# Optimization experiments

Hardware: AMD Instinct MI355X
Metric: run time of the kernel (lower is better)

## Reference

```python
import jax, jax.numpy as jnp
import numpy as np

B, T, D = 2, 2048, 1024
H = 16
HD = D // H  # 64
A = 16
MLP_H = 4 * D
EPS = 1e-6


def rmsnorm(x, w):
    # x: [..., C], w: [C]
    return x * jax.lax.rsqrt(jnp.mean(x * x, axis=-1, keepdims=True) + EPS) * w


def setup_inputs() -> dict:
    key = jax.random.key(0)
    ks = jax.random.split(key, 24)
    s = 0.02
    inp = {
        'x': jax.random.normal(ks[0], (B, T, D), jnp.float32),
        'actions': jax.random.normal(ks[1], (B, T, A), jnp.float32),
        # block norms
        'n1_w': jnp.ones((D,), jnp.float32),
        'n2_w': jnp.ones((D,), jnp.float32),
        # attention projections (stored [in, out])
        'q_w': jax.random.normal(ks[2], (D, D), jnp.float32) * s,
        'q_b': jnp.zeros((D,), jnp.float32),
        'k_w': jax.random.normal(ks[3], (D, D), jnp.float32) * s,
        'k_b': jnp.zeros((D,), jnp.float32),
        'v_w': jax.random.normal(ks[4], (D, D), jnp.float32) * s,
        'v_b': jnp.zeros((D,), jnp.float32),
        'qn_w': jnp.ones((HD,), jnp.float32),
        'kn_w': jnp.ones((HD,), jnp.float32),
        'o_w': jax.random.normal(ks[5], (D, D), jnp.float32) * s,
        'o_b': jnp.zeros((D,), jnp.float32),
        # action conditioning
        'ae1_w': jax.random.normal(ks[6], (A, D), jnp.float32) * s,
        'ae1_b': jnp.zeros((D,), jnp.float32),
        'ae2_w': jax.random.normal(ks[7], (D, D), jnp.float32) * s,
        'ae2_b': jnp.zeros((D,), jnp.float32),
        'mod_w': jax.random.normal(ks[8], (D, 4 * D), jnp.float32) * s,
        'mod_b': jnp.zeros((4 * D,), jnp.float32),
        # mlp
        'm1_w': jax.random.normal(ks[9], (D, MLP_H), jnp.float32) * s,
        'm1_b': jnp.zeros((MLP_H,), jnp.float32),
        'm2_w': jax.random.normal(ks[10], (MLP_H, D), jnp.float32) * s,
        'm2_b': jnp.zeros((D,), jnp.float32),
    }
    return inp


def _forward(x, actions, n1_w, n2_w, q_w, q_b, k_w, k_b, v_w, v_b, qn_w, kn_w,
             o_w, o_b, ae1_w, ae1_b, ae2_w, ae2_b, mod_w, mod_b,
             m1_w, m1_b, m2_w, m2_b):
    Bc, Tc, Dc = x.shape
    scale = HD ** -0.5

    # --- causal temporal attention with QK RMSNorm ---
    h = rmsnorm(x, n1_w)
    q = (h @ q_w + q_b).reshape(Bc, Tc, H, HD).transpose(0, 2, 1, 3)  # [B,H,T,hd]
    k = (h @ k_w + k_b).reshape(Bc, Tc, H, HD).transpose(0, 2, 1, 3)
    v = (h @ v_w + v_b).reshape(Bc, Tc, H, HD).transpose(0, 2, 1, 3)
    q = rmsnorm(q, qn_w)
    k = rmsnorm(k, kn_w)
    attn = jnp.einsum('bhqd,bhkd->bhqk', q, k) * scale
    causal = jnp.triu(jnp.ones((Tc, Tc), bool), k=1)  # True above diagonal -> masked
    attn = jnp.where(causal, -jnp.inf, attn)
    attn = jax.nn.softmax(attn, axis=-1)
    out = jnp.einsum('bhqk,bhkd->bhqd', attn, v)
    out = out.transpose(0, 2, 1, 3).reshape(Bc, Tc, Dc)
    x = x + (out @ o_w + o_b)

    # --- action conditioning (AdaLN-style; eval mode, no dropout) ---
    ae = jax.nn.silu(actions @ ae1_w + ae1_b) @ ae2_w + ae2_b  # [B,T,D]
    mod = jax.nn.silu(ae) @ mod_w + mod_b  # [B,T,4D]
    shift1, scale1, _, _ = jnp.split(mod, 4, axis=-1)
    x = x * (1.0 + scale1) + shift1

    # --- MLP ---
    h2 = rmsnorm(x, n2_w)
    x = x + (jax.nn.gelu(h2 @ m1_w + m1_b, approximate=False) @ m2_w + m2_b)
    return x


def reference(x, actions, n1_w, n2_w, q_w, q_b, k_w, k_b, v_w, v_b, qn_w, kn_w,
              o_w, o_b, ae1_w, ae1_b, ae2_w, ae2_b, mod_w, mod_b,
              m1_w, m1_b, m2_w, m2_b):
    return _forward(x, actions, n1_w, n2_w, q_w, q_b, k_w, k_b, v_w, v_b,
                    qn_w, kn_w, o_w, o_b, ae1_w, ae1_b, ae2_w, ae2_b,
                    mod_w, mod_b, m1_w, m1_b, m2_w, m2_b)
```

## Files before the change

kernel.cpp:

```cpp
#include <hip/hip_runtime.h>
#include <hip/hip_bf16.h>
#include <math.h>

typedef __hip_bfloat16 bf16;
typedef __attribute__((ext_vector_type(8))) short short8;
typedef __attribute__((ext_vector_type(4))) float float4_;

#define B_   2
#define T_   2048
#define D_   1024
#define H_   16
#define NTOK (B_ * T_)
#define NEG_SENT -1e30f

#define AS1 __attribute__((address_space(1)))
#define AS3 __attribute__((address_space(3)))

static __device__ __forceinline__ float b2f(bf16 v) { return __bfloat162float(v); }
static __device__ __forceinline__ bf16  f2b(float v) { return __float2bfloat16(v); }
static __device__ __forceinline__ short f2s(float v) {
    unsigned u = __builtin_bit_cast(unsigned, v);
    unsigned r = (u + 0x7FFFu + ((u >> 16) & 1u)) >> 16;
    return (short)r;
}
static __device__ __forceinline__ float to_f(float v) { return v; }
static __device__ __forceinline__ float to_f(bf16 v) { return __bfloat162float(v); }
static __device__ __forceinline__ void  store_o(float* p, float v) { *p = v; }
static __device__ __forceinline__ void  store_o(bf16* p, float v) { *p = __float2bfloat16(v); }
static __device__ __forceinline__ void gl_lds16(const void* g, void* l) {
    __builtin_amdgcn_global_load_lds((const AS1 unsigned int*)g, (AS3 unsigned int*)l, 16, 0, 0);
}

__global__ __launch_bounds__(256) void rmsnorm_k(const float* __restrict__ x,
                                                 const float* __restrict__ w,
                                                 bf16* __restrict__ out) {
    int t = blockIdx.x, tid = threadIdx.x;
    float xs[4], ss = 0.f;
#pragma unroll
    for (int i = 0; i < 4; ++i) {
        float v = x[(size_t)t * D_ + tid + i * 256];
        xs[i] = v; ss += v * v;
    }
    __shared__ float red[4];
#pragma unroll
    for (int off = 32; off > 0; off >>= 1) ss += __shfl_xor(ss, off, 64);
    if ((tid & 63) == 0) red[tid >> 6] = ss;
    __syncthreads();
    ss = red[0] + red[1] + red[2] + red[3];
    float inv = rsqrtf(ss * (1.f / D_) + 1e-6f);
#pragma unroll
    for (int i = 0; i < 4; ++i) {
        int c = tid + i * 256;
        out[(size_t)t * D_ + c] = f2b(xs[i] * inv * w[c]);
    }
}

__global__ __launch_bounds__(256) void modnorm_k(float* __restrict__ x1,
                                                 const bf16* __restrict__ mod,
                                                 const float* __restrict__ w,
                                                 bf16* __restrict__ h2) {
    int t = blockIdx.x, tid = threadIdx.x;
    float xs[4], ss = 0.f;
#pragma unroll
    for (int i = 0; i < 4; ++i) {
        int c = tid + i * 256;
        float sh = b2f(mod[(size_t)t * 2048 + c]);
        float sc = b2f(mod[(size_t)t * 2048 + 1024 + c]);
        float v = x1[(size_t)t * D_ + c] * (1.f + sc) + sh;
        xs[i] = v; ss += v * v;
        x1[(size_t)t * D_ + c] = v;
    }
    __shared__ float red[4];
#pragma unroll
    for (int off = 32; off > 0; off >>= 1) ss += __shfl_xor(ss, off, 64);
    if ((tid & 63) == 0) red[tid >> 6] = ss;
    __syncthreads();
    ss = red[0] + red[1] + red[2] + red[3];
    float inv = rsqrtf(ss * (1.f / D_) + 1e-6f);
#pragma unroll
    for (int i = 0; i < 4; ++i) {
        int c = tid + i * 256;
        h2[(size_t)t * D_ + c] = f2b(xs[i] * inv * w[c]);
    }
}

__global__ __launch_bounds__(256) void ae1_k(const float* __restrict__ actions,
                                             const float* __restrict__ w,
                                             const float* __restrict__ b,
                                             bf16* __restrict__ out) {
    int t = blockIdx.x, tid = threadIdx.x;
    float av[16];
#pragma unroll
    for (int a = 0; a < 16; ++a) av[a] = actions[(size_t)t * 16 + a];
#pragma unroll
    for (int i = 0; i < 4; ++i) {
        int n = tid + i * 256;
        float acc = b[n];
#pragma unroll
        for (int a = 0; a < 16; ++a) acc += av[a] * w[a * D_ + n];
        out[(size_t)t * D_ + n] = f2b(acc / (1.f + expf(-acc)));
    }
}

struct WD { const float* src; bf16* dst; int K, N, ldw, tiles; };
struct WPack { WD d[8]; };
__global__ __launch_bounds__(256) void wprep_k(WPack p) {
    int bid = blockIdx.x;
    int mi = 0, cum = 0;
#pragma unroll
    for (mi = 0; mi < 8; ++mi) {
        if (bid < cum + p.d[mi].tiles) break;
        cum += p.d[mi].tiles;
    }
    if (mi >= 8) return;
    WD w = p.d[mi];
    int local = bid - cum;
    int tilesK = w.K >> 6;
    int tk = local % tilesK, tn = local / tilesK;
    int k0 = tk * 64, n0 = tn * 64;
    __shared__ short Tt[64 * 72];
    int t = threadIdx.x;
    int row = t >> 2, seg = t & 3;
    const float* sp = w.src + (size_t)(k0 + row) * w.ldw + n0 + seg * 16;
#pragma unroll
    for (int q = 0; q < 4; ++q) {
        float4_ f = *(const float4_*)(sp + q * 4);
#pragma unroll
        for (int j = 0; j < 4; ++j) Tt[(seg * 16 + q * 4 + j) * 72 + row] = f2s(f[j]);
    }
    __syncthreads();
    bf16* dp = w.dst + (size_t)(n0 + row) * w.K + k0 + seg * 16;
    *(short8*)dp       = *(const short8*)&Tt[row * 72 + seg * 16];
    *(short8*)(dp + 8) = *(const short8*)&Tt[row * 72 + seg * 16 + 8];
}

__global__ __launch_bounds__(256) void bcat_k(const float* __restrict__ qb,
                                              const float* __restrict__ kb,
                                              const float* __restrict__ vb,
                                              float* __restrict__ dst) {
    int i = blockIdx.x * 256 + threadIdx.x;
    const float* s = (i < 1024) ? qb : (i < 2048) ? kb : vb;
    dst[i] = s[i & 1023];
}

template <int ACT, int QKN, typename ResT, typename OutT>
__global__ __launch_bounds__(256) void gemm_k(const bf16* __restrict__ A,
                                              const bf16* __restrict__ Bt,
                                              const float* __restrict__ bias,
                                              const ResT* __restrict__ res,
                                              OutT* __restrict__ out,
                                              int M, int N, int K, int ldo,
                                              const float* __restrict__ qn_w,
                                              const float* __restrict__ kn_w) {
    __shared__ __align__(16) short As[128 * 64];
    __shared__ __align__(16) short Bs[128 * 64];
    const int tid = threadIdx.x;
    const int bm = blockIdx.y * 128, bn = blockIdx.x * 128;
    const int wave = tid >> 6, lane = tid & 63;
    const int wm = (wave & 1) * 64, wn = (wave >> 1) * 64;
    const int l15 = lane & 15, quad = lane >> 4;
    const int lrow = lane >> 3, lseg = (lane & 7) * 8;
    float4_ acc[4][4] = {};

    for (int k0 = 0; k0 < K; k0 += 64) {
#pragma unroll
        for (int it = 0; it < 4; ++it) {
            int r = it * 32 + wave * 8;
            gl_lds16((const short*)A + (size_t)(bm + r + lrow) * K + k0 + lseg, &As[r * 64]);
            gl_lds16((const short*)Bt + (size_t)(bn + r + lrow) * K + k0 + lseg, &Bs[r * 64]);
        }
        __syncthreads();
#pragma unroll
        for (int kk = 0; kk < 64; kk += 32) {
            short8 af[4], bfr[4];
#pragma unroll
            for (int i = 0; i < 4; ++i)
                af[i] = *(const short8*)&As[(wm + i * 16 + l15) * 64 + kk + quad * 8];
#pragma unroll
            for (int j = 0; j < 4; ++j)
                bfr[j] = *(const short8*)&Bs[(wn + j * 16 + l15) * 64 + kk + quad * 8];
#pragma unroll
            for (int i = 0; i < 4; ++i)
#pragma unroll
                for (int j = 0; j < 4; ++j)
                    acc[i][j] = __builtin_amdgcn_mfma_f32_16x16x32_bf16(af[i], bfr[j], acc[i][j], 0, 0, 0);
        }
        __syncthreads();
    }

    int seg = (bn + wn) >> 10;
    float nwv[4];
    if (QKN && seg < 2) {
        const float* nw = seg ? kn_w : qn_w;
#pragma unroll
        for (int j = 0; j < 4; ++j) nwv[j] = nw[j * 16 + l15];
    }

#pragma unroll
    for (int i = 0; i < 4; ++i) {
        float vv[4][4];
#pragma unroll
        for (int j = 0; j < 4; ++j) {
            float bv = bias[bn + wn + j * 16 + l15];
#pragma unroll
            for (int r = 0; r < 4; ++r) vv[j][r] = acc[i][j][r] + bv;
        }
        if (QKN && seg < 2) {
#pragma unroll
            for (int r = 0; r < 4; ++r) {
                float ss = vv[0][r] * vv[0][r] + vv[1][r] * vv[1][r]
                         + vv[2][r] * vv[2][r] + vv[3][r] * vv[3][r];
#pragma unroll
                for (int off = 8; off > 0; off >>= 1) ss += __shfl_xor(ss, off, 16);
                float inv = rsqrtf(ss * (1.f / 64.f) + 1e-6f);
#pragma unroll
                for (int j = 0; j < 4; ++j) vv[j][r] *= inv * nwv[j];
            }
        }
#pragma unroll
        for (int j = 0; j < 4; ++j) {
            int col = bn + wn + j * 16 + l15;
#pragma unroll
            for (int r = 0; r < 4; ++r) {
                int row = bm + wm + i * 16 + quad * 4 + r;
                float v = vv[j][r];
                if (ACT == 1) v = v / (1.f + expf(-v));
                else if (ACT == 2) v = 0.5f * v * (1.f + erff(v * 0.70710678118654752f));
                if (res) v += to_f(res[(size_t)row * ldo + col]);
                store_o(&out[(size_t)row * ldo + col], v);
            }
        }
    }
}

template <int ACT, typename ResT, typename OutT>
__global__ __launch_bounds__(256) void gemm64_k(const bf16* __restrict__ A,
                                                const bf16* __restrict__ Bt,
                                                const float* __restrict__ bias,
                                                const ResT* __restrict__ res,
                                                OutT* __restrict__ out,
                                                int M, int N, int K) {
    __shared__ __align__(16) short As[64 * 64];
    __shared__ __align__(16) short Bs[128 * 64];
    const int tid = threadIdx.x;
    const int bm = blockIdx.y * 64, bn = blockIdx.x * 128;
    const int wave = tid >> 6, lane = tid & 63;
    const int wm = (wave & 1) * 32, wn = (wave >> 1) * 64;
    const int l15 = lane & 15, quad = lane >> 4;
    const int lrow = lane >> 3, lseg = (lane & 7) * 8;
    float4_ acc[2][4] = {};

    for (int k0 = 0; k0 < K; k0 += 64) {
#pragma unroll
        for (int it = 0; it < 2; ++it) {
            int r = wave * 16 + it * 8;
            gl_lds16((const short*)A + (size_t)(bm + r + lrow) * K + k0 + lseg, &As[r * 64]);
        }
#pragma unroll
        for (int it = 0; it < 4; ++it) {
            int r = it * 32 + wave * 8;
            gl_lds16((const short*)Bt + (size_t)(bn + r + lrow) * K + k0 + lseg, &Bs[r * 64]);
        }
        __syncthreads();
#pragma unroll
        for (int kk = 0; kk < 64; kk += 32) {
            short8 af[2], bfr[4];
#pragma unroll
            for (int i = 0; i < 2; ++i)
                af[i] = *(const short8*)&As[(wm + i * 16 + l15) * 64 + kk + quad * 8];
#pragma unroll
            for (int j = 0; j < 4; ++j)
                bfr[j] = *(const short8*)&Bs[(wn + j * 16 + l15) * 64 + kk + quad * 8];
#pragma unroll
            for (int i = 0; i < 2; ++i)
#pragma unroll
                for (int j = 0; j < 4; ++j)
                    acc[i][j] = __builtin_amdgcn_mfma_f32_16x16x32_bf16(af[i], bfr[j], acc[i][j], 0, 0, 0);
        }
        __syncthreads();
    }

#pragma unroll
    for (int i = 0; i < 2; ++i)
#pragma unroll
        for (int j = 0; j < 4; ++j) {
            int col = bn + wn + j * 16 + l15;
            float bv = bias[col];
#pragma unroll
            for (int r = 0; r < 4; ++r) {
                int row = bm + wm + i * 16 + quad * 4 + r;
                float v = acc[i][j][r] + bv;
                if (ACT == 1) v = v / (1.f + expf(-v));
                else if (ACT == 2) v = 0.5f * v * (1.f + erff(v * 0.70710678118654752f));
                if (res) v += to_f(res[(size_t)row * N + col]);
                store_o(&out[(size_t)row * N + col], v);
            }
        }
}

__global__ __launch_bounds__(256) void attn_k(const bf16* __restrict__ QKV,
                                              bf16* __restrict__ O) {
    __shared__ __align__(16) short Vt[2][64 * 72];
    __shared__ __align__(16) short Ps[4][16 * 72];
    const int bh = blockIdx.y, b = bh >> 4, h = bh & 15;
    const int q0 = T_ - 64 * (blockIdx.x + 1);
    const int tid = threadIdx.x, wave = tid >> 6, lane = tid & 63;
    const int l15 = lane & 15, quad = lane >> 4;
    const size_t base = (size_t)b * T_ * 3072 + h * 64;
    const short* Qp = (const short*)QKV + base;
    const short* Kp = Qp + 1024;
    const short* Vp = Qp + 2048;

    const int qrow = q0 + wave * 16 + l15;
    short8 qf0 = *(const short8*)(Qp + (size_t)qrow * 3072 + quad * 8);
    short8 qf1 = *(const short8*)(Qp + (size_t)qrow * 3072 + 32 + quad * 8);

    float4_ oacc[4] = {};
    float l_r[4] = {0.f, 0.f, 0.f, 0.f};

    const int vrow = tid >> 2, vseg = tid & 3;
    const int nit = q0 / 64 + 1;

    {
        const short* vp = Vp + (size_t)vrow * 3072 + vseg * 16;
        short8 v0 = *(const short8*)vp;
        short8 v1 = *(const short8*)(vp + 8);
#pragma unroll
        for (int j = 0; j < 8; ++j) Vt[0][(vseg * 16 + j) * 72 + vrow] = v0[j];
#pragma unroll
        for (int j = 0; j < 8; ++j) Vt[0][(vseg * 16 + 8 + j) * 72 + vrow] = v1[j];
    }
    __syncthreads();

    for (int it = 0; it < nit; ++it) {
        const int kv0 = it * 64, buf = it & 1;
        if (it + 1 < nit) {
            const short* vp = Vp + (size_t)(kv0 + 64 + vrow) * 3072 + vseg * 16;
            short8 v0 = *(const short8*)vp;
            short8 v1 = *(const short8*)(vp + 8);
#pragma unroll
            for (int j = 0; j < 8; ++j) Vt[buf ^ 1][(vseg * 16 + j) * 72 + vrow] = v0[j];
#pragma unroll
            for (int j = 0; j < 8; ++j) Vt[buf ^ 1][(vseg * 16 + 8 + j) * 72 + vrow] = v1[j];
        }

        float4_ s[4];
#pragma unroll
        for (int c = 0; c < 4; ++c) {
            const short* kp = Kp + (size_t)(kv0 + c * 16 + l15) * 3072 + quad * 8;
            short8 kb0 = *(const short8*)kp;
            short8 kb1 = *(const short8*)(kp + 32);
            float4_ sc = {};
            sc = __builtin_amdgcn_mfma_f32_16x16x32_bf16(qf0, kb0, sc, 0, 0, 0);
            sc = __builtin_amdgcn_mfma_f32_16x16x32_bf16(qf1, kb1, sc, 0, 0, 0);
            s[c] = sc;
        }

#pragma unroll
        for (int r = 0; r < 4; ++r) {
            int qr = q0 + wave * 16 + quad * 4 + r;
#pragma unroll
            for (int c = 0; c < 4; ++c) {
                int kvi = kv0 + c * 16 + l15;
                float val = (kvi > qr) ? NEG_SENT : s[c][r] * 0.125f;
                float p = __expf(val);
                s[c][r] = p;
                l_r[r] += p;
            }
        }

#pragma unroll
        for (int c = 0; c < 4; ++c)
#pragma unroll
            for (int r = 0; r < 4; ++r)
                Ps[wave][(quad * 4 + r) * 72 + c * 16 + l15] = f2s(s[c][r]);

#pragma unroll
        for (int kk = 0; kk < 64; kk += 32) {
            short8 pf = *(const short8*)&Ps[wave][l15 * 72 + kk + quad * 8];
#pragma unroll
            for (int d = 0; d < 4; ++d) {
                short8 vf = *(const short8*)&Vt[buf][(d * 16 + l15) * 72 + kk + quad * 8];
                oacc[d] = __builtin_amdgcn_mfma_f32_16x16x32_bf16(pf, vf, oacc[d], 0, 0, 0);
            }
        }
        __syncthreads();
    }

    float linv[4];
#pragma unroll
    for (int r = 0; r < 4; ++r) {
        float l = l_r[r];
#pragma unroll
        for (int off = 8; off > 0; off >>= 1) l += __shfl_xor(l, off, 16);
        linv[r] = 1.f / l;
    }
#pragma unroll
    for (int d = 0; d < 4; ++d)
#pragma unroll
        for (int r = 0; r < 4; ++r) {
            int qr = q0 + wave * 16 + quad * 4 + r;
            O[(size_t)(b * T_ + qr) * D_ + h * 64 + d * 16 + l15] = f2b(oacc[d][r] * linv[r]);
        }
}

extern "C" void kernel_launch(void* const* d_in, const int* in_sizes, int n_in,
                              void* d_out, int out_size, void* d_ws, size_t ws_size,
                              hipStream_t stream) {
    const float* x     = (const float*)d_in[0];
    const float* acts  = (const float*)d_in[1];
    const float* n1_w  = (const float*)d_in[2];
    const float* n2_w  = (const float*)d_in[3];
    const float* q_w   = (const float*)d_in[4];
    const float* q_b   = (const float*)d_in[5];
    const float* k_w   = (const float*)d_in[6];
    const float* k_b   = (const float*)d_in[7];
    const float* v_w   = (const float*)d_in[8];
    const float* v_b   = (const float*)d_in[9];
    const float* qn_w  = (const float*)d_in[10];
    const float* kn_w  = (const float*)d_in[11];
    const float* o_w   = (const float*)d_in[12];
    const float* o_b   = (const float*)d_in[13];
    const float* ae1_w = (const float*)d_in[14];
    const float* ae1_b = (const float*)d_in[15];
    const float* ae2_w = (const float*)d_in[16];
    const float* ae2_b = (const float*)d_in[17];
    const float* mod_w = (const float*)d_in[18];
    const float* mod_b = (const float*)d_in[19];
    const float* m1_w  = (const float*)d_in[20];
    const float* m1_b  = (const float*)d_in[21];
    const float* m2_w  = (const float*)d_in[22];
    const float* m2_b  = (const float*)d_in[23];
    float* out = (float*)d_out;

    char* ws = (char*)d_ws;
    const size_t MB = 1ull << 20;
    bf16*  Ah   = (bf16*)(ws + 0);
    bf16*  QKVp = (bf16*)(ws + 8 * MB);
    bf16*  AO   = (bf16*)(ws + 32 * MB);
    bf16*  AE1  = (bf16*)(ws + 8 * MB);
    bf16*  AES  = (bf16*)(ws + 16 * MB);
    bf16*  MOD  = (bf16*)(ws + 24 * MB);
    bf16*  M1G  = (bf16*)(ws + 8 * MB);
    float* X1   = out;

    bf16* WTqkv = (bf16*)(ws + 40 * MB);
    bf16* WTo   = (bf16*)(ws + 46 * MB);
    bf16* WTae2 = (bf16*)(ws + 48 * MB);
    bf16* WTmod = (bf16*)(ws + 50 * MB);
    bf16* WTm1  = (bf16*)(ws + 54 * MB);
    bf16* WTm2  = (bf16*)(ws + 62 * MB);
    float* biasQKV = (float*)(ws + 70 * MB);

    dim3 blk(256);

    WPack p;
    p.d[0] = { q_w,   WTqkv,                1024, 1024, 1024, 256 };
    p.d[1] = { k_w,   WTqkv + 1024 * 1024,  1024, 1024, 1024, 256 };
    p.d[2] = { v_w,   WTqkv + 2048 * 1024,  1024, 1024, 1024, 256 };
    p.d[3] = { o_w,   WTo,   1024, 1024, 1024, 256 };
    p.d[4] = { ae2_w, WTae2, 1024, 1024, 1024, 256 };
    p.d[5] = { mod_w, WTmod, 1024, 2048, 4096, 512 };
    p.d[6] = { m1_w,  WTm1,  1024, 4096, 4096, 1024 };
    p.d[7] = { m2_w,  WTm2,  4096, 1024, 1024, 1024 };
    wprep_k<<<3840, blk, 0, stream>>>(p);
    bcat_k<<<12, blk, 0, stream>>>(q_b, k_b, v_b, biasQKV);

    rmsnorm_k<<<NTOK, blk, 0, stream>>>(x, n1_w, Ah);
    gemm_k<0, 1, float, bf16><<<dim3(24, 32), blk, 0, stream>>>(Ah, WTqkv, biasQKV, (const float*)nullptr, QKVp, NTOK, 3072, 1024, 3072, qn_w, kn_w);
    attn_k<<<dim3(T_ / 64, B_ * H_), blk, 0, stream>>>(QKVp, AO);
    gemm64_k<0, float, float><<<dim3(8, 64), blk, 0, stream>>>(AO, WTo, o_b, x, X1, NTOK, 1024, 1024);
    ae1_k<<<NTOK, blk, 0, stream>>>(acts, ae1_w, ae1_b, AE1);
    gemm64_k<1, float, bf16><<<dim3(8, 64), blk, 0, stream>>>(AE1, WTae2, ae2_b, (const float*)nullptr, AES, NTOK, 1024, 1024);
    gemm_k<0, 0, float, bf16><<<dim3(16, 32), blk, 0, stream>>>(AES, WTmod, mod_b, (const float*)nullptr, MOD, NTOK, 2048, 1024, 2048, nullptr, nullptr);
    modnorm_k<<<NTOK, blk, 0, stream>>>(X1, MOD, n2_w, Ah);
    gemm_k<2, 0, float, bf16><<<dim3(32, 32), blk, 0, stream>>>(Ah, WTm1, m1_b, (const float*)nullptr, M1G, NTOK, 4096, 1024, 4096, nullptr, nullptr);
    gemm64_k<0, float, float><<<dim3(8, 64), blk, 0, stream>>>(M1G, WTm2, m2_b, X1, out, NTOK, 1024, 4096);
}
```

Baseline: 594.1 us.

## Write V transposed from QKV GEMM and use single-wave attention blocks

The QKV GEMM epilogue now writes V directly in a head-major transposed layout [b,h,d,t] and Q/K into a 2048-wide buffer. The attention kernel drops its LDS transpose of V, double buffering and block syncs, and reads V fragments straight from global memory. It also switches to one 64-thread wave per 16 query rows, giving four times as many blocks. This removes the in-kernel transpose and barrier cost, but V is now reloaded from global/L2 by each wave instead of being shared through LDS across four waves.

```diff
diff --git a/kernel.cpp b/kernel.cpp
--- a/kernel.cpp
+++ b/kernel.cpp
@@ -5,6 +5,7 @@
 typedef __hip_bfloat16 bf16;
 typedef __attribute__((ext_vector_type(8))) short short8;
 typedef __attribute__((ext_vector_type(4))) float float4_;
+typedef __attribute__((ext_vector_type(4))) unsigned short ushort4_;
 
 #define B_   2
 #define T_   2048
@@ -18,10 +19,10 @@
 
 static __device__ __forceinline__ float b2f(bf16 v) { return __bfloat162float(v); }
 static __device__ __forceinline__ bf16  f2b(float v) { return __float2bfloat16(v); }
-static __device__ __forceinline__ short f2s(float v) {
+static __device__ __forceinline__ unsigned short f2s(float v) {
     unsigned u = __builtin_bit_cast(unsigned, v);
     unsigned r = (u + 0x7FFFu + ((u >> 16) & 1u)) >> 16;
-    return (short)r;
+    return (unsigned short)r;
 }
 static __device__ __forceinline__ float to_f(float v) { return v; }
 static __device__ __forceinline__ float to_f(bf16 v) { return __bfloat162float(v); }
@@ -126,7 +127,7 @@
     for (int q = 0; q < 4; ++q) {
         float4_ f = *(const float4_*)(sp + q * 4);
 #pragma unroll
-        for (int j = 0; j < 4; ++j) Tt[(seg * 16 + q * 4 + j) * 72 + row] = f2s(f[j]);
+        for (int j = 0; j < 4; ++j) Tt[(seg * 16 + q * 4 + j) * 72 + row] = (short)f2s(f[j]);
     }
     __syncthreads();
     bf16* dp = w.dst + (size_t)(n0 + row) * w.K + k0 + seg * 16;
@@ -143,7 +144,7 @@
     dst[i] = s[i & 1023];
 }
 
-template <int ACT, int QKN, typename ResT, typename OutT>
+template <int ACT, int QKN, int VOUT, typename ResT, typename OutT>
 __global__ __launch_bounds__(256) void gemm_k(const bf16* __restrict__ A,
                                               const bf16* __restrict__ Bt,
                                               const float* __restrict__ bias,
@@ -151,7 +152,8 @@
                                               OutT* __restrict__ out,
                                               int M, int N, int K, int ldo,
                                               const float* __restrict__ qn_w,
-                                              const float* __restrict__ kn_w) {
+                                              const float* __restrict__ kn_w,
+                                              bf16* __restrict__ vt) {
     __shared__ __align__(16) short As[128 * 64];
     __shared__ __align__(16) short Bs[128 * 64];
     const int tid = threadIdx.x;
@@ -217,17 +219,29 @@
                 for (int j = 0; j < 4; ++j) vv[j][r] *= inv * nwv[j];
             }
         }
-#pragma unroll
-        for (int j = 0; j < 4; ++j) {
-            int col = bn + wn + j * 16 + l15;
-#pragma unroll
-            for (int r = 0; r < 4; ++r) {
-                int row = bm + wm + i * 16 + quad * 4 + r;
-                float v = vv[j][r];
-                if (ACT == 1) v = v / (1.f + expf(-v));
-                else if (ACT == 2) v = 0.5f * v * (1.f + erff(v * 0.70710678118654752f));
-                if (res) v += to_f(res[(size_t)row * ldo + col]);
-                store_o(&out[(size_t)row * ldo + col], v);
+        if (VOUT && seg >= 2) {
+#pragma unroll
+            for (int j = 0; j < 4; ++j) {
+                int col = bn + wn + j * 16 + l15 - 2048;
+                int hh = col >> 6, hd = col & 63;
+                int row0 = bm + wm + i * 16 + quad * 4;
+                int bb = row0 >> 11, t0 = row0 & 2047;
+                ushort4_ u = { f2s(vv[j][0]), f2s(vv[j][1]), f2s(vv[j][2]), f2s(vv[j][3]) };
+                *(ushort4_*)((unsigned short*)vt + ((size_t)((bb * 16 + hh) * 64 + hd)) * 2048 + t0) = u;
+            }
+        } else {
+#pragma unroll
+            for (int j = 0; j < 4; ++j) {
+                int col = bn + wn + j * 16 + l15;
+#pragma unroll
+                for (int r = 0; r < 4; ++r) {
+                    int row = bm + wm + i * 16 + quad * 4 + r;
+                    float v = vv[j][r];
+                    if (ACT == 1) v = v / (1.f + expf(-v));
+                    else if (ACT == 2) v = 0.5f * v * (1.f + erff(v * 0.70710678118654752f));
+                    if (res) v += to_f(res[(size_t)row * ldo + col]);
+                    store_o(&out[(size_t)row * ldo + col], v);
+                }
             }
         }
     }
@@ -298,56 +312,33 @@
         }
 }
 
-__global__ __launch_bounds__(256) void attn_k(const bf16* __restrict__ QKV,
-                                              bf16* __restrict__ O) {
-    __shared__ __align__(16) short Vt[2][64 * 72];
-    __shared__ __align__(16) short Ps[4][16 * 72];
+__global__ __launch_bounds__(64) void attn_k(const bf16* __restrict__ QK,
+                                             const bf16* __restrict__ VT,
+                                             bf16* __restrict__ O) {
+    __shared__ __align__(16) short Ps[16 * 72];
     const int bh = blockIdx.y, b = bh >> 4, h = bh & 15;
-    const int q0 = T_ - 64 * (blockIdx.x + 1);
-    const int tid = threadIdx.x, wave = tid >> 6, lane = tid & 63;
+    const int q0 = T_ - 16 * (blockIdx.x + 1);
+    const int lane = threadIdx.x;
     const int l15 = lane & 15, quad = lane >> 4;
-    const size_t base = (size_t)b * T_ * 3072 + h * 64;
-    const short* Qp = (const short*)QKV + base;
+    const short* Qp = (const short*)QK + (size_t)b * T_ * 2048 + h * 64;
     const short* Kp = Qp + 1024;
-    const short* Vp = Qp + 2048;
-
-    const int qrow = q0 + wave * 16 + l15;
-    short8 qf0 = *(const short8*)(Qp + (size_t)qrow * 3072 + quad * 8);
-    short8 qf1 = *(const short8*)(Qp + (size_t)qrow * 3072 + 32 + quad * 8);
+    const short* Vp = (const short*)VT + (size_t)(b * 16 + h) * 64 * 2048;
+
+    const int qrow = q0 + l15;
+    short8 qf0 = *(const short8*)(Qp + (size_t)qrow * 2048 + quad * 8);
+    short8 qf1 = *(const short8*)(Qp + (size_t)qrow * 2048 + 32 + quad * 8);
 
     float4_ oacc[4] = {};
     float l_r[4] = {0.f, 0.f, 0.f, 0.f};
-
-    const int vrow = tid >> 2, vseg = tid & 3;
     const int nit = q0 / 64 + 1;
 
-    {
-        const short* vp = Vp + (size_t)vrow * 3072 + vseg * 16;
-        short8 v0 = *(const short8*)vp;
-        short8 v1 = *(const short8*)(vp + 8);
-#pragma unroll
-        for (int j = 0; j < 8; ++j) Vt[0][(vseg * 16 + j) * 72 + vrow] = v0[j];
-#pragma unroll
-        for (int j = 0; j < 8; ++j) Vt[0][(vseg * 16 + 8 + j) * 72 + vrow] = v1[j];
-    }
-    __syncthreads();
-
     for (int it = 0; it < nit; ++it) {
-        const int kv0 = it * 64, buf = it & 1;
-        if (it + 1 < nit) {
-            const short* vp = Vp + (size_t)(kv0 + 64 + vrow) * 3072 + vseg * 16;
-            short8 v0 = *(const short8*)vp;
-            short8 v1 = *(const short8*)(vp + 8);
-#pragma unroll
-            for (int j = 0; j < 8; ++j) Vt[buf ^ 1][(vseg * 16 + j) * 72 + vrow] = v0[j];
-#pragma unroll
-            for (int j = 0; j < 8; ++j) Vt[buf ^ 1][(vseg * 16 + 8 + j) * 72 + vrow] = v1[j];
-        }
+        const int kv0 = it * 64;
 
         float4_ s[4];
 #pragma unroll
         for (int c = 0; c < 4; ++c) {
-            const short* kp = Kp + (size_t)(kv0 + c * 16 + l15) * 3072 + quad * 8;
+            const short* kp = Kp + (size_t)(kv0 + c * 16 + l15) * 2048 + quad * 8;
             short8 kb0 = *(const short8*)kp;
             short8 kb1 = *(const short8*)(kp + 32);
             float4_ sc = {};
@@ -358,7 +349,7 @@
 
 #pragma unroll
         for (int r = 0; r < 4; ++r) {
-            int qr = q0 + wave * 16 + quad * 4 + r;
+            int qr = q0 + quad * 4 + r;
 #pragma unroll
             for (int c = 0; c < 4; ++c) {
                 int kvi = kv0 + c * 16 + l15;
@@ -373,18 +364,17 @@
         for (int c = 0; c < 4; ++c)
 #pragma unroll
             for (int r = 0; r < 4; ++r)
-                Ps[wave][(quad * 4 + r) * 72 + c * 16 + l15] = f2s(s[c][r]);
+                Ps[(quad * 4 + r) * 72 + c * 16 + l15] = (short)f2s(s[c][r]);
 
 #pragma unroll
         for (int kk = 0; kk < 64; kk += 32) {
-            short8 pf = *(const short8*)&Ps[wave][l15 * 72 + kk + quad * 8];
+            short8 pf = *(const short8*)&Ps[l15 * 72 + kk + quad * 8];
 #pragma unroll
             for (int d = 0; d < 4; ++d) {
-                short8 vf = *(const short8*)&Vt[buf][(d * 16 + l15) * 72 + kk + quad * 8];
+                short8 vf = *(const short8*)(Vp + (size_t)(d * 16 + l15) * 2048 + kv0 + kk + quad * 8);
                 oacc[d] = __builtin_amdgcn_mfma_f32_16x16x32_bf16(pf, vf, oacc[d], 0, 0, 0);
             }
         }
-        __syncthreads();
     }
 
     float linv[4];
@@ -399,7 +389,7 @@
     for (int d = 0; d < 4; ++d)
 #pragma unroll
         for (int r = 0; r < 4; ++r) {
-            int qr = q0 + wave * 16 + quad * 4 + r;
+            int qr = q0 + quad * 4 + r;
             O[(size_t)(b * T_ + qr) * D_ + h * 64 + d * 16 + l15] = f2b(oacc[d][r] * linv[r]);
         }
 }
@@ -436,7 +426,8 @@
     char* ws = (char*)d_ws;
     const size_t MB = 1ull << 20;
     bf16*  Ah   = (bf16*)(ws + 0);
-    bf16*  QKVp = (bf16*)(ws + 8 * MB);
+    bf16*  QKp  = (bf16*)(ws + 8 * MB);
+    bf16*  VT   = (bf16*)(ws + 24 * MB);
     bf16*  AO   = (bf16*)(ws + 32 * MB);
     bf16*  AE1  = (bf16*)(ws + 8 * MB);
     bf16*  AES  = (bf16*)(ws + 16 * MB);
@@ -467,13 +458,13 @@
     bcat_k<<<12, blk, 0, stream>>>(q_b, k_b, v_b, biasQKV);
 
     rmsnorm_k<<<NTOK, blk, 0, stream>>>(x, n1_w, Ah);
-    gemm_k<0, 1, float, bf16><<<dim3(24, 32), blk, 0, stream>>>(Ah, WTqkv, biasQKV, (const float*)nullptr, QKVp, NTOK, 3072, 1024, 3072, qn_w, kn_w);
-    attn_k<<<dim3(T_ / 64, B_ * H_), blk, 0, stream>>>(QKVp, AO);
+    gemm_k<0, 1, 1, float, bf16><<<dim3(24, 32), blk, 0, stream>>>(Ah, WTqkv, biasQKV, (const float*)nullptr, QKp, NTOK, 3072, 1024, 2048, qn_w, kn_w, VT);
+    attn_k<<<dim3(T_ / 16, B_ * H_), dim3(64), 0, stream>>>(QKp, VT, AO);
     gemm64_k<0, float, float><<<dim3(8, 64), blk, 0, stream>>>(AO, WTo, o_b, x, X1, NTOK, 1024, 1024);
     ae1_k<<<NTOK, blk, 0, stream>>>(acts, ae1_w, ae1_b, AE1);
     gemm64_k<1, float, bf16><<<dim3(8, 64), blk, 0, stream>>>(AE1, WTae2, ae2_b, (const float*)nullptr, AES, NTOK, 1024, 1024);
-    gemm_k<0, 0, float, bf16><<<dim3(16, 32), blk, 0, stream>>>(AES, WTmod, mod_b, (const float*)nullptr, MOD, NTOK, 2048, 1024, 2048, nullptr, nullptr);
+    gemm_k<0, 0, 0, float, bf16><<<dim3(16, 32), blk, 0, stream>>>(AES, WTmod, mod_b, (const float*)nullptr, MOD, NTOK, 2048, 1024, 2048, nullptr, nullptr, nullptr);
     modnorm_k<<<NTOK, blk, 0, stream>>>(X1, MOD, n2_w, Ah);
-    gemm_k<2, 0, float, bf16><<<dim3(32, 32), blk, 0, stream>>>(Ah, WTm1, m1_b, (const float*)nullptr, M1G, NTOK, 4096, 1024, 4096, nullptr, nullptr);
+    gemm_k<2, 0, 0, float, bf16><<<dim3(32, 32), blk, 0, stream>>>(Ah, WTm1, m1_b, (const float*)nullptr, M1G, NTOK, 4096, 1024, 4096, nullptr, nullptr, nullptr);
     gemm64_k<0, float, float><<<dim3(8, 64), blk, 0, stream>>>(M1G, WTm2, m2_b, X1, out, NTOK, 1024, 4096);
 }
```

Measured after the change: 690.4 us. 16.2% more time.
